# Optimization experiments

Hardware: AMD Instinct MI355X
Metric: run time of the kernel (lower is better)

## Reference

```python
import jax, jax.numpy as jnp
import numpy as np

COST_CENTER = 1.0
COST_GIOU = 2.0
BIG = jnp.float32(1e9)


def _lsa(cost, nrows):
    """Exact rectangular linear sum assignment (Jonker-Volgenant shortest
    augmenting path, same algorithm as scipy.optimize.linear_sum_assignment).
    cost: [m, n] with m <= n. Only the first `nrows` rows are assigned.
    Returns col4row [m] int32: assigned column per row (-1 for inactive rows)."""
    m, n = cost.shape

    def augment_row(i, state):
        def do_aug(state):
            u, v, row4col, col4row = state
            init = (jnp.int32(-1), jnp.int32(i), jnp.float32(0.0),
                    jnp.full((n,), BIG, jnp.float32),      # shortest path costs
                    jnp.full((n,), -1, jnp.int32),          # predecessor row per col
                    jnp.zeros((n,), bool),                  # scanned columns SC
                    jnp.zeros((m,), bool))                  # scanned rows SR

            def cond(c):
                return c[0] < 0  # until a free column (sink) is found

            def body(c):
                sink, cur, minval, shortest, path, SC, SR = c
                SR = SR.at[cur].set(True)
                red = minval + cost[cur] - u[cur] - v       # reduced costs [n]
                better = (~SC) & (red < shortest)
                shortest = jnp.where(better, red, shortest)
                path = jnp.where(better, cur, path)
                cand = jnp.where(SC, BIG, shortest)
                j = jnp.argmin(cand).astype(jnp.int32)
                minval = cand[j]
                SC = SC.at[j].set(True)
                r = row4col[j]
                free = r < 0
                sink = jnp.where(free, j, jnp.int32(-1))
                cur = jnp.where(free, cur, r)
                return (sink, cur, minval, shortest, path, SC, SR)

            sink, _, minval, shortest, path, SC, SR = jax.lax.while_loop(cond, body, init)

            # dual (potential) updates, exactly as scipy's rectangular_lsap
            u = u.at[i].add(minval)
            rows = jnp.arange(m)
            sr_other = SR & (rows != i)
            u = jnp.where(sr_other, u + minval - shortest[jnp.clip(col4row, 0, n - 1)], u)
            v = jnp.where(SC, v - (minval - shortest), v)

            # augment: flip the alternating path from sink back to row i
            def acond(c):
                return ~c[0]

            def abody(c):
                done, j, row4col, col4row = c
                r = path[j]
                row4col = row4col.at[j].set(r)
                jnext = col4row[r]
                col4row = col4row.at[r].set(j)
                return (r == i, jnext, row4col, col4row)

            _, _, row4col, col4row = jax.lax.while_loop(
                acond, abody, (jnp.bool_(False), sink, row4col, col4row))
            return (u, v, row4col, col4row)

        return jax.lax.cond(i < nrows, do_aug, lambda s: s, state)

    state = (jnp.zeros((m,), jnp.float32), jnp.zeros((n,), jnp.float32),
             jnp.full((n,), -1, jnp.int32), jnp.full((m,), -1, jnp.int32))
    _, _, _, col4row = jax.lax.fori_loop(0, m, augment_row, state)
    return col4row


def _match(center_dist, gious, nactual_gt):
    # final_cost = cost_center * center_dist + cost_giou * (-gious)  [B, P, G]
    cost = COST_CENTER * center_dist - COST_GIOU * gious
    B, P, G = cost.shape
    costT = jnp.transpose(cost, (0, 2, 1))               # [B, G, P]: rows=GT, cols=proposals
    col4row = jax.vmap(_lsa)(costT, nactual_gt)          # [B, G] proposal index per GT

    gt_ids = jnp.arange(G, dtype=jnp.int32)[None, :]     # [1, G]
    valid = gt_ids < nactual_gt[:, None]
    props = jnp.where(valid, col4row, jnp.int32(P))      # invalid -> OOB, dropped
    b_ids = jnp.arange(B)[:, None]
    per_prop_gt_inds = jnp.zeros((B, P), jnp.int32).at[b_ids, props].set(
        jnp.broadcast_to(gt_ids, (B, G)), mode='drop')
    proposal_matched_mask = jnp.zeros((B, P), jnp.float32).at[b_ids, props].set(
        1.0, mode='drop')
    return per_prop_gt_inds, proposal_matched_mask


def setup_inputs() -> dict:
    key = jax.random.key(0)
    k1, k2, k3 = jax.random.split(key, 3)
    B, P, G = 8, 4096, 96
    center_dist = jax.random.uniform(k1, (B, P, G), jnp.float32) * 10.0
    gious = jax.random.uniform(k2, (B, P, G), jnp.float32) * 2.0 - 1.0  # gIoU in [-1, 1]
    nactual_gt = jax.random.randint(k3, (B,), 0, G + 1).astype(jnp.int32)
    return {"center_dist": center_dist, "gious": gious, "nactual_gt": nactual_gt}


def reference(center_dist, gious, nactual_gt):
    return _match(center_dist, gious, nactual_gt)
```

## Files before the change

kernel.cpp:

```cpp
#include <hip/hip_runtime.h>
#include <hip/hip_bf16.h>


#define P_N 4096
#define G_M 96
#define BIGF 1e9f
#define NSTRIPE 64

__device__ __forceinline__ void lexmin(float& bv, int& bi, float ov, int oi) {
    if (ov < bv || (ov == bv && oi < bi)) { bv = ov; bi = oi; }
}
__device__ __forceinline__ unsigned int ord32(float f) {
    unsigned int u = __float_as_uint(f);
    return u ^ ((unsigned int)((int)u >> 31) | 0x80000000u);
}
__device__ __forceinline__ float unord32(unsigned int k) {
    unsigned int u = (k & 0x80000000u) ? (k ^ 0x80000000u) : ~k;
    return __uint_as_float(u);
}

#define DPP_I(x, ctrl) __builtin_amdgcn_update_dpp(x, x, ctrl, 0xF, 0xF, false)
__device__ __forceinline__ float wave_min_f32(float x) {
    x = fminf(x, __int_as_float(DPP_I(__float_as_int(x), 0xB1)));
    x = fminf(x, __int_as_float(DPP_I(__float_as_int(x), 0x4E)));
    x = fminf(x, __int_as_float(DPP_I(__float_as_int(x), 0x141)));
    x = fminf(x, __int_as_float(DPP_I(__float_as_int(x), 0x140)));
    x = fminf(x, __int_as_float(__builtin_amdgcn_ds_swizzle(__float_as_int(x), 0x401F)));
    x = fminf(x, __shfl_xor(x, 32, 64));
    return x;
}
__device__ __forceinline__ int wave_min_i32(int x) {
    x = min(x, DPP_I(x, 0xB1));
    x = min(x, DPP_I(x, 0x4E));
    x = min(x, DPP_I(x, 0x141));
    x = min(x, DPP_I(x, 0x140));
    x = min(x, __builtin_amdgcn_ds_swizzle(x, 0x401F));
    x = min(x, __shfl_xor(x, 32, 64));
    return x;
}

__global__ __launch_bounds__(256) void cost_prep(
    const float* __restrict__ cd, const float* __restrict__ gi,
    const int* __restrict__ nactual,
    float* __restrict__ costT, unsigned long long* __restrict__ partial)
{
    __shared__ float tile[64][G_M + 1];
    const int b  = blockIdx.x >> 6;
    const int st = blockIdx.x & 63;
    const int pb = st * 64;
    const int nrows = nactual[b];
    if (nrows <= 0) return;

    const size_t base = ((size_t)b * P_N + pb) * G_M;
    for (int t = threadIdx.x; t < 64 * nrows; t += 256) {
        int p = t / nrows, g = t - p * nrows;
        size_t idx = base + (size_t)p * G_M + g;
        tile[p][g] = cd[idx] - 2.0f * gi[idx];
    }
    __syncthreads();
    for (int t = threadIdx.x; t < nrows * 64; t += 256) {
        int g = t >> 6, p = t & 63;
        costT[((size_t)b * G_M + g) * P_N + pb + p] = tile[p][g];
    }
    if (threadIdx.x < nrows) {
        int g = threadIdx.x;
        float bv = tile[0][g]; int bp = pb;
        #pragma unroll 8
        for (int p = 1; p < 64; ++p) {
            float val = tile[p][g];
            if (val < bv) { bv = val; bp = pb + p; }
        }
        partial[((size_t)b * NSTRIPE + st) * G_M + g] =
            ((unsigned long long)ord32(bv) << 32) | (unsigned int)bp;
    }
}

__global__ __launch_bounds__(256, 1) void lsa_solve(
    const float* __restrict__ costT,
    const unsigned long long* __restrict__ partial,
    const int* __restrict__ nactual,
    float* __restrict__ out, int B)
{
    const int b = blockIdx.x;
    const int tid = threadIdx.x;
    const int lane = tid & 63;
    const int wave = tid >> 6;

    __shared__ float shL[P_N];
    __shared__ unsigned int prL[P_N / 4];
    __shared__ short row4col[P_N];
    __shared__ unsigned long long cand[4][G_M];
    __shared__ float u[G_M];
    __shared__ short col4row[G_M];
    __shared__ short argcL[G_M];
    __shared__ short pend[G_M];
    __shared__ int s_npend, s_sink, s_i;
    __shared__ float s_minval;
    __shared__ unsigned long long s_SR0, s_SR1;

    const int nrows = nactual[b];

    #pragma unroll
    for (int k = 0; k < 4; ++k) {
        int c = k * 1024 + tid * 4;
        *(uint2*)&row4col[c] = make_uint2(0xFFFFFFFFu, 0xFFFFFFFFu);
        *(int4*)&shL[c] = make_int4(0x7FFFFFFF, 0x7FFFFFFF, 0x7FFFFFFF, 0x7FFFFFFF);
    }
    if (tid < G_M) col4row[tid] = -1;
    if (tid == 0) s_npend = 0;

    if (nrows > 0) {
        const unsigned long long* pbase = partial + (size_t)b * NSTRIPE * G_M;
        unsigned long long b1 = ~0ull, b2 = ~0ull;
        #pragma unroll 4
        for (int s = 0; s < 16; ++s) {
            const unsigned long long* row = pbase + (size_t)(wave * 16 + s) * G_M;
            unsigned long long p1 = row[lane];
            if (p1 < b1) b1 = p1;
            if (lane < 32) {
                unsigned long long p2 = row[64 + lane];
                if (p2 < b2) b2 = p2;
            }
        }
        cand[wave][lane] = b1;
        if (lane < 32) cand[wave][64 + lane] = b2;
    }
    __syncthreads();
    if (wave == 0 && nrows > 0) {
        #pragma unroll
        for (int r0 = 0; r0 < G_M; r0 += 64) {
            int r = r0 + lane;
            if (r < G_M) {
                unsigned long long best = cand[0][r];
                if (cand[1][r] < best) best = cand[1][r];
                if (cand[2][r] < best) best = cand[2][r];
                if (cand[3][r] < best) best = cand[3][r];
                u[r] = unord32((unsigned int)(best >> 32));
                argcL[r] = (short)(best & 0xFFFFull);
            }
        }
    }
    __syncthreads();

    int* claim = (int*)shL;
    const int r1 = lane, r2 = 64 + lane;
    const bool a1 = (wave == 0) && (r1 < nrows);
    const bool a2 = (wave == 0) && (r2 < G_M) && (r2 < nrows);
    const int j1 = a1 ? argcL[r1] : 0, j2 = a2 ? argcL[r2] : 0;
    if (a1) atomicMin(&claim[j1], r1);
    if (a2) atomicMin(&claim[j2], r2);
    __syncthreads();
    if (wave == 0) {
        const bool w1 = a1 && (*(volatile int*)&claim[j1] == r1);
        const bool w2 = a2 && (*(volatile int*)&claim[j2] == r2);
        unsigned long long l1 = __ballot(a1 && !w1);
        unsigned long long l2 = __ballot(a2 && !w2);
        if (w1) { row4col[j1] = (short)r1; col4row[r1] = (short)j1; }
        if (w2) { row4col[j2] = (short)r2; col4row[r2] = (short)j2; }
        const int n1 = __popcll(l1);
        const unsigned long long below = (1ull << lane) - 1;
        if (a1 && !w1) pend[__popcll(l1 & below)] = (short)r1;
        if (a2 && !w2) pend[n1 + __popcll(l2 & below)] = (short)r2;
        if (lane == 0) s_npend = n1 + __popcll(l2);
    }
    __syncthreads();
    const int npend = s_npend;

    float4 vr[16], shr[16];
    unsigned int pr[16];
    unsigned long long scm = 0;
    const float4 BIG4 = make_float4(BIGF, BIGF, BIGF, BIGF);
    #pragma unroll
    for (int k = 0; k < 16; ++k) {
        vr[k] = make_float4(0.f, 0.f, 0.f, 0.f);
        shr[k] = BIG4; pr[k] = 0u;
    }

    for (int pi = 0; pi < npend; ++pi) {
        if (wave == 0) {
            const int i = pend[pi];
            float minval = 0.0f;
            int cur = i, sink = -1;
            unsigned long long SR0 = 0, SR1 = 0;

            for (int guard = 0; guard <= P_N; ++guard) {
                if (cur < 64) SR0 |= 1ull << cur; else SR1 |= 1ull << (cur - 64);
                const float ucur = u[cur];
                const float4* crow4 =
                    (const float4*)(costT + ((size_t)b * G_M + cur) * P_N);

                float bv = 3.0e38f; int bi = P_N;
                #pragma unroll
                for (int k = 0; k < 16; ++k) {
                    const float4 cc = crow4[k * 64 + lane];
                    float4 sh = shr[k];
                    const float4 vv = vr[k];
                    const unsigned int mb = (unsigned int)(scm >> (k * 4)) & 0xFu;
                    float q0 = ((minval + cc.x) - ucur) - vv.x;
                    float q1 = ((minval + cc.y) - ucur) - vv.y;
                    float q2 = ((minval + cc.z) - ucur) - vv.z;
                    float q3 = ((minval + cc.w) - ucur) - vv.w;
                    const bool u0 = !(mb & 1u), u1 = !(mb & 2u);
                    const bool u2 = !(mb & 4u), u3 = !(mb & 8u);
                    if (u0 && q0 < sh.x) { sh.x = q0; pr[k] = (pr[k] & 0xFFFFFF00u) | (unsigned)cur; }
                    if (u1 && q1 < sh.y) { sh.y = q1; pr[k] = (pr[k] & 0xFFFF00FFu) | ((unsigned)cur << 8); }
                    if (u2 && q2 < sh.z) { sh.z = q2; pr[k] = (pr[k] & 0xFF00FFFFu) | ((unsigned)cur << 16); }
                    if (u3 && q3 < sh.w) { sh.w = q3; pr[k] = (pr[k] & 0x00FFFFFFu) | ((unsigned)cur << 24); }
                    shr[k] = sh;
                    const int cbase = k * 256 + lane * 4;
                    lexmin(bv, bi, u0 ? sh.x : BIGF, cbase + 0);
                    lexmin(bv, bi, u1 ? sh.y : BIGF, cbase + 1);
                    lexmin(bv, bi, u2 ? sh.z : BIGF, cbase + 2);
                    lexmin(bv, bi, u3 ? sh.w : BIGF, cbase + 3);
                }
                const float gv = wave_min_f32(bv);
                const int gidx = wave_min_i32(bv == gv ? bi : 0x7FFFFFFF);
                minval = gv;
                if (gidx >= P_N) { sink = -2; break; }
                if (((gidx >> 2) & 63) == lane)
                    scm |= 1ull << (((gidx >> 8) << 2) | (gidx & 3));
                const int r = row4col[gidx];
                if (r < 0) { sink = gidx; break; }
                cur = r;
            }
            if (lane == 0) {
                s_sink = sink; s_minval = minval; s_i = i;
                s_SR0 = SR0; s_SR1 = SR1;
            }
        }
        __syncthreads();
        const int sink = s_sink;
        const float minval = s_minval;
        const int i = s_i;

        if (wave == 0 && sink >= 0) {
            #pragma unroll
            for (int k = 0; k < 16; ++k) {
                const int c = k * 256 + lane * 4;
                *(float4*)&shL[c] = shr[k];
                prL[k * 64 + lane] = pr[k];
            }
        }
        __syncthreads();
        if (sink >= 0 && tid < G_M) {
            const bool sr = (tid < 64) ? ((s_SR0 >> tid) & 1ull)
                                       : ((s_SR1 >> (tid - 64)) & 1ull);
            if (tid == i) u[tid] = u[tid] + minval;
            else if (sr) {
                int c4 = col4row[tid]; if (c4 < 0) c4 = 0;
                u[tid] = (u[tid] + minval) - shL[c4];
            }
        }
        __syncthreads();
        if (wave == 0 && sink >= 0) {
            #pragma unroll
            for (int k = 0; k < 16; ++k) {
                const unsigned int mb = (unsigned int)(scm >> (k * 4)) & 0xFu;
                float4 vv = vr[k];
                const float4 sh = shr[k];
                if (mb & 1u) vv.x -= minval - sh.x;
                if (mb & 2u) vv.y -= minval - sh.y;
                if (mb & 4u) vv.z -= minval - sh.z;
                if (mb & 8u) vv.w -= minval - sh.w;
                vr[k] = vv;
                shr[k] = BIG4;
            }
            scm = 0;
            if (lane == 0) {
                int j = sink;
                for (int g2 = 0; g2 < G_M + 2; ++g2) {
                    int r = (int)((prL[j >> 2] >> (8 * (j & 3))) & 0xFFu);
                    row4col[j] = (short)r;
                    int jn = col4row[r];
                    col4row[r] = (short)j;
                    if (r == i) break;
                    j = jn;
                }
            }
        }
        __syncthreads();
    }

    float* out_inds = out + (size_t)b * P_N;
    float* out_mask = out + (size_t)B * P_N + (size_t)b * P_N;
    #pragma unroll
    for (int k = 0; k < 4; ++k) {
        int c = k * 1024 + tid * 4;
        uint2 rr = *(const uint2*)&row4col[c];
        short q0 = (short)(rr.x & 0xFFFFu), q1 = (short)(rr.x >> 16);
        short q2 = (short)(rr.y & 0xFFFFu), q3 = (short)(rr.y >> 16);
        float4 fi, fm;
        fi.x = q0 >= 0 ? (float)q0 : 0.f;  fm.x = q0 >= 0 ? 1.f : 0.f;
        fi.y = q1 >= 0 ? (float)q1 : 0.f;  fm.y = q1 >= 0 ? 1.f : 0.f;
        fi.z = q2 >= 0 ? (float)q2 : 0.f;  fm.z = q2 >= 0 ? 1.f : 0.f;
        fi.w = q3 >= 0 ? (float)q3 : 0.f;  fm.w = q3 >= 0 ? 1.f : 0.f;
        *(float4*)&out_inds[c] = fi;
        *(float4*)&out_mask[c] = fm;
    }
}

#define BLK 1024
#define WAVES (BLK / 64)
__global__ __launch_bounds__(BLK) void lsa_full(
    const float* __restrict__ cd, const float* __restrict__ gi,
    const int* __restrict__ nactual,
    float* __restrict__ out, int B)
{
    const int b = blockIdx.x, tid = threadIdx.x;
    __shared__ float v[P_N];
    __shared__ float shortest[P_N];
    __shared__ short path[P_N];
    __shared__ short row4col[P_N];
    __shared__ unsigned char SC[P_N];
    __shared__ float u[G_M];
    __shared__ short col4row[G_M];
    __shared__ unsigned char SR[G_M];
    __shared__ float s_minval;
    __shared__ int s_j, s_cur, s_done;
    __shared__ float rv[WAVES];
    __shared__ int ri[WAVES];

    for (int j = tid; j < P_N; j += BLK) { v[j] = 0.0f; row4col[j] = -1; }
    if (tid < G_M) { u[tid] = 0.0f; col4row[tid] = -1; }
    const int nrows = nactual[b];
    __syncthreads();

    for (int i = 0; i < nrows; ++i) {
        for (int j = tid; j < P_N; j += BLK) { shortest[j] = BIGF; path[j] = -1; SC[j] = 0; }
        if (tid < G_M) SR[tid] = 0;
        if (tid == 0) s_done = 0;
        __syncthreads();
        float minval = 0.0f; int cur = i, sink = -1;
        while (true) {
            if (tid == 0) SR[cur] = 1;
            const float ucur = u[cur];
            #pragma unroll
            for (int k = 0; k < P_N / BLK; ++k) {
                int j = tid + k * BLK;
                if (!SC[j]) {
                    size_t idx = ((size_t)b * P_N + j) * G_M + cur;
                    float c = cd[idx] - 2.0f * gi[idx];
                    float red = ((minval + c) - ucur) - v[j];
                    if (red < shortest[j]) { shortest[j] = red; path[j] = (short)cur; }
                }
            }
            __syncthreads();
            float bv = 3.0e38f; int bi = P_N;
            #pragma unroll
            for (int k = 0; k < P_N / BLK; ++k) {
                int j = tid + k * BLK;
                lexmin(bv, bi, SC[j] ? BIGF : shortest[j], j);
            }
            #pragma unroll
            for (int off = 32; off > 0; off >>= 1) {
                float ov = __shfl_xor(bv, off, 64);
                int oi = __shfl_xor(bi, off, 64);
                lexmin(bv, bi, ov, oi);
            }
            if ((tid & 63) == 0) { rv[tid >> 6] = bv; ri[tid >> 6] = bi; }
            __syncthreads();
            if (tid == 0) {
                float mv = rv[0]; int mi = ri[0];
                for (int w = 1; w < WAVES; ++w) lexmin(mv, mi, rv[w], ri[w]);
                s_minval = mv; s_j = mi; SC[mi] = 1;
                int r = row4col[mi];
                if (r < 0) s_done = 1; else s_cur = r;
            }
            __syncthreads();
            minval = s_minval;
            if (s_done) { sink = s_j; break; }
            cur = s_cur;
        }
        if (tid < G_M) {
            if (tid == i) u[tid] += minval;
            else if (SR[tid]) {
                int c = col4row[tid]; if (c < 0) c = 0;
                u[tid] = (u[tid] + minval) - shortest[c];
            }
        }
        #pragma unroll
        for (int k = 0; k < P_N / BLK; ++k) {
            int j = tid + k * BLK;
            if (SC[j]) v[j] -= (minval - shortest[j]);
        }
        __syncthreads();
        if (tid == 0) {
            int j = sink;
            while (true) {
                int r = path[j];
                row4col[j] = (short)r;
                int jn = col4row[r];
                col4row[r] = (short)j;
                if (r == i) break;
                j = jn;
            }
        }
        __syncthreads();
    }
    float* out_inds = out + (size_t)b * P_N;
    float* out_mask = out + (size_t)B * P_N + (size_t)b * P_N;
    for (int j = tid; j < P_N; j += BLK) {
        int r = row4col[j];
        out_inds[j] = (r >= 0) ? (float)r : 0.0f;
        out_mask[j] = (r >= 0) ? 1.0f : 0.0f;
    }
}

extern "C" void kernel_launch(void* const* d_in, const int* in_sizes, int n_in,
                              void* d_out, int out_size, void* d_ws, size_t ws_size,
                              hipStream_t stream) {
    const float* cd = (const float*)d_in[0];
    const float* gi = (const float*)d_in[1];
    const int*   na = (const int*)d_in[2];
    float* out = (float*)d_out;
    const int B = in_sizes[2];

    const size_t costT_b = (size_t)B * G_M * P_N * sizeof(float);
    const size_t pm_b    = (size_t)B * NSTRIPE * G_M * sizeof(unsigned long long);
    auto al = [](size_t x) { return (x + 255) & ~(size_t)255; };
    const size_t o1 = al(costT_b);
    const size_t need = o1 + al(pm_b);

    if (ws_size >= need) {
        float* costT = (float*)d_ws;
        unsigned long long* pm = (unsigned long long*)((char*)d_ws + o1);
        cost_prep<<<dim3(B * NSTRIPE), 256, 0, stream>>>(cd, gi, na, costT, pm);
        lsa_solve<<<dim3(B), 256, 0, stream>>>(costT, pm, na, out, B);
    } else {
        lsa_full<<<dim3(B), BLK, 0, stream>>>(cd, gi, na, out, B);
    }
}
```

Baseline: 101.7 us.

## Split LSA augmenting-path scan across four waves and vectorize cost prep loads

The shortest-augmenting-path inner loop now spreads the 4096 columns over all four waves instead of only wave 0. Each wave reduces its own argmin and the waves combine through a double-buffered shared array, with one barrier per path step. Scanned columns are now tracked with an additive BIG mask register rather than a bitmask, and predecessor rows are stored per lane. The cost prep kernel also switches to float4 loads over all 96 columns regardless of nrows. The main cost removed is serial per-step work in a single wave, paid for with a block-wide barrier on every step. The loop guard is also lowered from P_N to G_M.

```diff
diff --git a/kernel.cpp b/kernel.cpp
--- a/kernel.cpp
+++ b/kernel.cpp
@@ -52,23 +52,34 @@
     if (nrows <= 0) return;
 
     const size_t base = ((size_t)b * P_N + pb) * G_M;
-    for (int t = threadIdx.x; t < 64 * nrows; t += 256) {
-        int p = t / nrows, g = t - p * nrows;
-        size_t idx = base + (size_t)p * G_M + g;
-        tile[p][g] = cd[idx] - 2.0f * gi[idx];
+    const int p   = threadIdx.x >> 2;
+    const int sub = threadIdx.x & 3;
+    {
+        const float* crow = cd + base + (size_t)p * G_M + sub * 24;
+        const float* grow = gi + base + (size_t)p * G_M + sub * 24;
+        #pragma unroll
+        for (int j = 0; j < 6; ++j) {
+            const float4 a = *(const float4*)(crow + 4 * j);
+            const float4 g = *(const float4*)(grow + 4 * j);
+            const int g0 = sub * 24 + 4 * j;
+            tile[p][g0 + 0] = a.x - 2.0f * g.x;
+            tile[p][g0 + 1] = a.y - 2.0f * g.y;
+            tile[p][g0 + 2] = a.z - 2.0f * g.z;
+            tile[p][g0 + 3] = a.w - 2.0f * g.w;
+        }
     }
     __syncthreads();
     for (int t = threadIdx.x; t < nrows * 64; t += 256) {
-        int g = t >> 6, p = t & 63;
-        costT[((size_t)b * G_M + g) * P_N + pb + p] = tile[p][g];
+        int g = t >> 6, pp = t & 63;
+        costT[((size_t)b * G_M + g) * P_N + pb + pp] = tile[pp][g];
     }
     if (threadIdx.x < nrows) {
         int g = threadIdx.x;
         float bv = tile[0][g]; int bp = pb;
         #pragma unroll 8
-        for (int p = 1; p < 64; ++p) {
-            float val = tile[p][g];
-            if (val < bv) { bv = val; bp = pb + p; }
+        for (int q = 1; q < 64; ++q) {
+            float val = tile[q][g];
+            if (val < bv) { bv = val; bp = pb + q; }
         }
         partial[((size_t)b * NSTRIPE + st) * G_M + g] =
             ((unsigned long long)ord32(bv) << 32) | (unsigned int)bp;
@@ -90,13 +101,12 @@
     __shared__ unsigned int prL[P_N / 4];
     __shared__ short row4col[P_N];
     __shared__ unsigned long long cand[4][G_M];
+    __shared__ unsigned long long scand[2][4];
     __shared__ float u[G_M];
     __shared__ short col4row[G_M];
     __shared__ short argcL[G_M];
     __shared__ short pend[G_M];
-    __shared__ int s_npend, s_sink, s_i;
-    __shared__ float s_minval;
-    __shared__ unsigned long long s_SR0, s_SR1;
+    __shared__ int s_npend;
 
     const int nrows = nactual[b];
 
@@ -166,85 +176,104 @@
     __syncthreads();
     const int npend = s_npend;
 
-    float4 vr[16], shr[16];
-    unsigned int pr[16];
-    unsigned long long scm = 0;
+    float4 vr[4], shr[4], mfr[4];
+    uint4 prv[4];
     const float4 BIG4 = make_float4(BIGF, BIGF, BIGF, BIGF);
+    const float4 Z4 = make_float4(0.f, 0.f, 0.f, 0.f);
     #pragma unroll
-    for (int k = 0; k < 16; ++k) {
-        vr[k] = make_float4(0.f, 0.f, 0.f, 0.f);
-        shr[k] = BIG4; pr[k] = 0u;
-    }
+    for (int k = 0; k < 4; ++k) {
+        vr[k] = Z4; shr[k] = BIG4; mfr[k] = Z4;
+        prv[k] = make_uint4(0u, 0u, 0u, 0u);
+    }
+
+    const float4* crowb = (const float4*)(costT + (size_t)b * G_M * P_N);
+    const int chunk = (wave << 8) + lane;
 
     for (int pi = 0; pi < npend; ++pi) {
-        if (wave == 0) {
-            const int i = pend[pi];
-            float minval = 0.0f;
-            int cur = i, sink = -1;
-            unsigned long long SR0 = 0, SR1 = 0;
-
-            for (int guard = 0; guard <= P_N; ++guard) {
-                if (cur < 64) SR0 |= 1ull << cur; else SR1 |= 1ull << (cur - 64);
-                const float ucur = u[cur];
-                const float4* crow4 =
-                    (const float4*)(costT + ((size_t)b * G_M + cur) * P_N);
-
-                float bv = 3.0e38f; int bi = P_N;
+        const int i = pend[pi];
+        float minval = 0.0f;
+        int cur = i, sink = -1, par = 0;
+        unsigned long long SR0 = 0ull, SR1 = 0ull;
+
+        for (int guard = 0; guard <= G_M; ++guard) {
+            if (cur < 64) SR0 |= 1ull << cur; else SR1 |= 1ull << (cur - 64);
+            const float mu = minval - u[cur];
+            const float4* crow4 = crowb + (size_t)cur * (P_N / 4);
+
+            float bv = 3.0e38f; int bi = 0x7FFFFFFF;
+            #pragma unroll
+            for (int k = 0; k < 4; ++k) {
+                const float4 cc = crow4[chunk + (k << 6)];
+                const float4 vv = vr[k];
+                const float4 mf = mfr[k];
+                float4 sh = shr[k];
+                uint4 pv = prv[k];
+                const int cb = (wave << 10) + (k << 8) + (lane << 2);
+                const float q0 = ((cc.x + mu) - vv.x) + mf.x;
+                const float q1 = ((cc.y + mu) - vv.y) + mf.y;
+                const float q2 = ((cc.z + mu) - vv.z) + mf.z;
+                const float q3 = ((cc.w + mu) - vv.w) + mf.w;
+                if (q0 < sh.x) { sh.x = q0; pv.x = (unsigned)cur; }
+                if (q1 < sh.y) { sh.y = q1; pv.y = (unsigned)cur; }
+                if (q2 < sh.z) { sh.z = q2; pv.z = (unsigned)cur; }
+                if (q3 < sh.w) { sh.w = q3; pv.w = (unsigned)cur; }
+                shr[k] = sh; prv[k] = pv;
+                const float s0 = sh.x + mf.x;
+                const float s1 = sh.y + mf.y;
+                const float s2 = sh.z + mf.z;
+                const float s3 = sh.w + mf.w;
+                if (s0 < bv) { bv = s0; bi = cb + 0; }
+                if (s1 < bv) { bv = s1; bi = cb + 1; }
+                if (s2 < bv) { bv = s2; bi = cb + 2; }
+                if (s3 < bv) { bv = s3; bi = cb + 3; }
+            }
+            const float gvw = wave_min_f32(bv);
+            const int giw = wave_min_i32(bv == gvw ? bi : 0x7FFFFFFF);
+            if (lane == 0)
+                scand[par][wave] =
+                    ((unsigned long long)ord32(gvw) << 32) | (unsigned int)giw;
+            __syncthreads();
+            unsigned long long best = scand[par][0];
+            unsigned long long t;
+            t = scand[par][1]; if (t < best) best = t;
+            t = scand[par][2]; if (t < best) best = t;
+            t = scand[par][3]; if (t < best) best = t;
+            const int gidx = (int)(best & 0xFFFFFFFFull);
+            minval = unord32((unsigned int)(best >> 32));
+            if (gidx >= P_N) { sink = -2; break; }
+            const int loc = gidx - (wave << 10);
+            if (loc >= 0 && loc < 1024 && ((loc >> 2) & 63) == lane) {
+                const int kk = loc >> 8, qq = loc & 3;
                 #pragma unroll
-                for (int k = 0; k < 16; ++k) {
-                    const float4 cc = crow4[k * 64 + lane];
-                    float4 sh = shr[k];
-                    const float4 vv = vr[k];
-                    const unsigned int mb = (unsigned int)(scm >> (k * 4)) & 0xFu;
-                    float q0 = ((minval + cc.x) - ucur) - vv.x;
-                    float q1 = ((minval + cc.y) - ucur) - vv.y;
-                    float q2 = ((minval + cc.z) - ucur) - vv.z;
-                    float q3 = ((minval + cc.w) - ucur) - vv.w;
-                    const bool u0 = !(mb & 1u), u1 = !(mb & 2u);
-                    const bool u2 = !(mb & 4u), u3 = !(mb & 8u);
-                    if (u0 && q0 < sh.x) { sh.x = q0; pr[k] = (pr[k] & 0xFFFFFF00u) | (unsigned)cur; }
-                    if (u1 && q1 < sh.y) { sh.y = q1; pr[k] = (pr[k] & 0xFFFF00FFu) | ((unsigned)cur << 8); }
-                    if (u2 && q2 < sh.z) { sh.z = q2; pr[k] = (pr[k] & 0xFF00FFFFu) | ((unsigned)cur << 16); }
-                    if (u3 && q3 < sh.w) { sh.w = q3; pr[k] = (pr[k] & 0x00FFFFFFu) | ((unsigned)cur << 24); }
-                    shr[k] = sh;
-                    const int cbase = k * 256 + lane * 4;
-                    lexmin(bv, bi, u0 ? sh.x : BIGF, cbase + 0);
-                    lexmin(bv, bi, u1 ? sh.y : BIGF, cbase + 1);
-                    lexmin(bv, bi, u2 ? sh.z : BIGF, cbase + 2);
-                    lexmin(bv, bi, u3 ? sh.w : BIGF, cbase + 3);
+                for (int k2 = 0; k2 < 4; ++k2) {
+                    if (k2 == kk) {
+                        if (qq == 0) mfr[k2].x = BIGF;
+                        else if (qq == 1) mfr[k2].y = BIGF;
+                        else if (qq == 2) mfr[k2].z = BIGF;
+                        else mfr[k2].w = BIGF;
+                    }
                 }
-                const float gv = wave_min_f32(bv);
-                const int gidx = wave_min_i32(bv == gv ? bi : 0x7FFFFFFF);
-                minval = gv;
-                if (gidx >= P_N) { sink = -2; break; }
-                if (((gidx >> 2) & 63) == lane)
-                    scm |= 1ull << (((gidx >> 8) << 2) | (gidx & 3));
-                const int r = row4col[gidx];
-                if (r < 0) { sink = gidx; break; }
-                cur = r;
-            }
-            if (lane == 0) {
-                s_sink = sink; s_minval = minval; s_i = i;
-                s_SR0 = SR0; s_SR1 = SR1;
-            }
-        }
-        __syncthreads();
-        const int sink = s_sink;
-        const float minval = s_minval;
-        const int i = s_i;
-
-        if (wave == 0 && sink >= 0) {
-            #pragma unroll
-            for (int k = 0; k < 16; ++k) {
-                const int c = k * 256 + lane * 4;
+            }
+            const int r = row4col[gidx];
+            if (r < 0) { sink = gidx; break; }
+            cur = r;
+            par ^= 1;
+        }
+
+        if (sink >= 0) {
+            #pragma unroll
+            for (int k = 0; k < 4; ++k) {
+                const int c = (wave << 10) + (k << 8) + (lane << 2);
                 *(float4*)&shL[c] = shr[k];
-                prL[k * 64 + lane] = pr[k];
+                const uint4 pv = prv[k];
+                prL[c >> 2] = (pv.x & 0xFFu) | ((pv.y & 0xFFu) << 8) |
+                              ((pv.z & 0xFFu) << 16) | ((pv.w & 0xFFu) << 24);
             }
         }
         __syncthreads();
         if (sink >= 0 && tid < G_M) {
-            const bool sr = (tid < 64) ? ((s_SR0 >> tid) & 1ull)
-                                       : ((s_SR1 >> (tid - 64)) & 1ull);
+            const bool sr = (tid < 64) ? ((SR0 >> tid) & 1ull)
+                                       : ((SR1 >> (tid - 64)) & 1ull);
             if (tid == i) u[tid] = u[tid] + minval;
             else if (sr) {
                 int c4 = col4row[tid]; if (c4 < 0) c4 = 0;
@@ -252,21 +281,20 @@
             }
         }
         __syncthreads();
-        if (wave == 0 && sink >= 0) {
-            #pragma unroll
-            for (int k = 0; k < 16; ++k) {
-                const unsigned int mb = (unsigned int)(scm >> (k * 4)) & 0xFu;
+        if (sink >= 0) {
+            #pragma unroll
+            for (int k = 0; k < 4; ++k) {
                 float4 vv = vr[k];
                 const float4 sh = shr[k];
-                if (mb & 1u) vv.x -= minval - sh.x;
-                if (mb & 2u) vv.y -= minval - sh.y;
-                if (mb & 4u) vv.z -= minval - sh.z;
-                if (mb & 8u) vv.w -= minval - sh.w;
+                const float4 mf = mfr[k];
+                if (mf.x > 0.f) vv.x -= minval - sh.x;
+                if (mf.y > 0.f) vv.y -= minval - sh.y;
+                if (mf.z > 0.f) vv.z -= minval - sh.z;
+                if (mf.w > 0.f) vv.w -= minval - sh.w;
                 vr[k] = vv;
-                shr[k] = BIG4;
-            }
-            scm = 0;
-            if (lane == 0) {
+                shr[k] = BIG4; mfr[k] = Z4;
+            }
+            if (tid == 0) {
                 int j = sink;
                 for (int g2 = 0; g2 < G_M + 2; ++g2) {
                     int r = (int)((prL[j >> 2] >> (8 * (j & 3))) & 0xFFu);
@@ -277,6 +305,9 @@
                     j = jn;
                 }
             }
+        } else {
+            #pragma unroll
+            for (int k = 0; k < 4; ++k) { shr[k] = BIG4; mfr[k] = Z4; }
         }
         __syncthreads();
     }
```

Result: faster. 85.14 us (-16.3%).
